# Kernel tuning notes

Hardware: AMD Instinct MI355X
Metric: run time of the kernel (lower is better)

Reference implementation:

```python
import jax, jax.numpy as jnp
import numpy as np

N_NODES = 40000
N_EDGES = 640000
D_IN = 512
D_OUT = 128


def setup_inputs() -> dict:
    key = jax.random.key(0)
    k_x, k_w, k_a, k_v, k_r, k_c = jax.random.split(key, 6)
    # Xavier-uniform bound for Linear(in=512, out=128)
    bound = float(np.sqrt(6.0 / (D_IN + D_OUT)))
    x = jax.random.normal(k_x, (N_NODES, D_IN), dtype=jnp.float32)
    weight = jax.random.uniform(k_w, (D_OUT, D_IN), dtype=jnp.float32,
                                minval=-bound, maxval=bound)
    bias = jnp.zeros((D_OUT,), dtype=jnp.float32)
    # PReLU default init is 0.25 (single shared slope)
    alpha = jnp.full((1,), 0.25, dtype=jnp.float32)
    edge_val = jax.random.uniform(k_v, (N_EDGES,), dtype=jnp.float32)
    edge_row = jax.random.randint(k_r, (N_EDGES,), 0, N_NODES, dtype=jnp.int32)
    edge_col = jax.random.randint(k_c, (N_EDGES,), 0, N_NODES, dtype=jnp.int32)
    return {"x": x, "weight": weight, "bias": bias, "alpha": alpha,
            "edge_val": edge_val, "edge_row": edge_row, "edge_col": edge_col}


def reference(x, weight, bias, alpha, edge_val, edge_row, edge_col):
    # seq = fc_1(input): [N, D_out]
    seq = jnp.einsum('ni,oi->no', x, weight)
    # torch.spmm(adj, seq) with adj in COO form:
    # out[r] = sum over edges (r, c, v) of v * seq[c]
    msgs = edge_val[:, None] * seq[edge_col]          # [E, D_out]
    agg = jax.ops.segment_sum(msgs, edge_row, num_segments=x.shape[0])
    agg = agg + bias
    # PReLU with a single shared slope alpha
    return jnp.where(agg > 0, agg, alpha[0] * agg)
```

## Files before the change

kernel.cpp:

```cpp
#include <hip/hip_runtime.h>
#include <hip/hip_bf16.h>

#define N_NODES 40000
#define N_EDGES 640000
#define D_IN 512
#define D_OUT 128
#define BM 128
#define BK 64
#define CAPC 32
#define OVF_MAX 4096
#define NB_GE 313
#define NB_SC 625
#define EPT 4

typedef __attribute__((ext_vector_type(4))) float f32x4;
typedef __attribute__((ext_vector_type(8))) short bf16x8;
typedef __attribute__((ext_vector_type(4))) unsigned short us4;

static __device__ __forceinline__ unsigned short f2bf(float f) {
    unsigned int u = __float_as_uint(f);
    unsigned int r = u + 0x7fffu + ((u >> 16) & 1u);
    return (unsigned short)(r >> 16);
}

__global__ __launch_bounds__(256) void prep_kernel(int4* __restrict__ zbase, int nz4)
{
    const int stride = 512 * 256;
    for (int i = blockIdx.x * 256 + threadIdx.x; i < nz4; i += stride)
        zbase[i] = make_int4(0, 0, 0, 0);
}

__global__ __launch_bounds__(256) void fused_kernel(
    const float* __restrict__ x, const float* __restrict__ w,
    unsigned short* __restrict__ seq,
    const int* __restrict__ erow, const int* __restrict__ ecol,
    const float* __restrict__ eval, int* __restrict__ cursor,
    unsigned int* __restrict__ bucket, int* __restrict__ ovf_cnt,
    int4* __restrict__ ovf)
{
    if (blockIdx.x >= NB_GE) {
        const int base = (blockIdx.x - NB_GE) * (256 * EPT) + threadIdx.x;
        int r[EPT], c[EPT];
        float v[EPT];
        #pragma unroll
        for (int j = 0; j < EPT; j++) {
            int e = base + j * 256;
            r[j] = erow[e]; c[j] = ecol[e]; v[j] = eval[e];
        }
        int slot[EPT];
        #pragma unroll
        for (int j = 0; j < EPT; j++) slot[j] = atomicAdd(&cursor[r[j]], 1);
        #pragma unroll
        for (int j = 0; j < EPT; j++) {
            if (slot[j] < CAPC) {
                bucket[(size_t)r[j] * CAPC + slot[j]] =
                    ((unsigned int)f2bf(v[j]) << 16) | (unsigned int)c[j];
            } else {
                int o = atomicAdd(ovf_cnt, 1);
                if (o < OVF_MAX)
                    ovf[o] = make_int4(r[j], c[j], __float_as_int(v[j]), 0);
            }
        }
        return;
    }

    __shared__ unsigned short As[BM * BK];
    __shared__ unsigned short Bs[D_OUT * BK];

    const int tid = threadIdx.x;
    const int lane = tid & 63;
    const int wv = tid >> 6;
    const int block_row = blockIdx.x * BM;
    const int srow = tid >> 3;
    const int scol = (tid & 7) * 8;

    f32x4 ra[4][2], rb[4][2];

    auto issue_loads = [&](int k0) {
        #pragma unroll
        for (int p = 0; p < 4; ++p) {
            int gr = block_row + srow + p * 32; if (gr >= N_NODES) gr = N_NODES - 1;
            const float* sa = x + (size_t)gr * D_IN + k0 + scol;
            ra[p][0] = *(const f32x4*)sa;
            ra[p][1] = *(const f32x4*)(sa + 4);
            const float* sb = w + (size_t)(srow + p * 32) * D_IN + k0 + scol;
            rb[p][0] = *(const f32x4*)sb;
            rb[p][1] = *(const f32x4*)(sb + 4);
        }
    };

    f32x4 acc[2][8];
    #pragma unroll
    for (int i = 0; i < 2; i++)
        #pragma unroll
        for (int j = 0; j < 8; j++)
            acc[i][j] = f32x4{0.f, 0.f, 0.f, 0.f};

    issue_loads(0);

    for (int kt = 0; kt < D_IN / BK; ++kt) {
        __syncthreads();
        #pragma unroll
        for (int p = 0; p < 4; ++p) {
            int r = srow + p * 32;
            us4 h0, h1, g0, g1;
            #pragma unroll
            for (int q = 0; q < 4; q++) {
                h0[q] = f2bf(ra[p][0][q]); h1[q] = f2bf(ra[p][1][q]);
                g0[q] = f2bf(rb[p][0][q]); g1[q] = f2bf(rb[p][1][q]);
            }
            int off = (r * (BK * 2) + scol * 2) ^ ((r & 7) << 4);
            *(us4*)((char*)As + off)     = h0;
            *(us4*)((char*)As + off + 8) = h1;
            *(us4*)((char*)Bs + off)     = g0;
            *(us4*)((char*)Bs + off + 8) = g1;
        }
        if (kt < D_IN / BK - 1) issue_loads((kt + 1) * BK);
        __syncthreads();

        #pragma unroll
        for (int ks = 0; ks < 2; ++ks) {
            const int kb = ks * 32 + (lane >> 4) * 8;
            bf16x8 a[2], b[8];
            #pragma unroll
            for (int m = 0; m < 2; m++) {
                int r = wv * 32 + m * 16 + (lane & 15);
                int off = (r * (BK * 2) + kb * 2) ^ ((r & 7) << 4);
                a[m] = *(const bf16x8*)((const char*)As + off);
            }
            #pragma unroll
            for (int n = 0; n < 8; n++) {
                int r = n * 16 + (lane & 15);
                int off = (r * (BK * 2) + kb * 2) ^ ((r & 7) << 4);
                b[n] = *(const bf16x8*)((const char*)Bs + off);
            }
            #pragma unroll
            for (int m = 0; m < 2; m++)
                #pragma unroll
                for (int n = 0; n < 8; n++)
                    acc[m][n] = __builtin_amdgcn_mfma_f32_16x16x32_bf16(a[m], b[n], acc[m][n], 0, 0, 0);
        }
    }

    #pragma unroll
    for (int m = 0; m < 2; m++) {
        #pragma unroll
        for (int r = 0; r < 4; r++) {
            int grow = block_row + wv * 32 + m * 16 + (lane >> 4) * 4 + r;
            if (grow < N_NODES) {
                #pragma unroll
                for (int n = 0; n < 8; n++) {
                    int col = n * 16 + (lane & 15);
                    seq[(size_t)grow * D_OUT + col] = f2bf(acc[m][n][r]);
                }
            }
        }
    }
}

__global__ __launch_bounds__(256) void agg_kernel(
    const unsigned short* __restrict__ seq, const int* __restrict__ cursor,
    const unsigned int* __restrict__ bucket, const int* __restrict__ ovf_cnt,
    const int4* __restrict__ ovf, const float* __restrict__ bias,
    const float* __restrict__ alpha, float* __restrict__ out)
{
    const int row = blockIdx.x * 4 + (threadIdx.x >> 6);
    const int lane = threadIdx.x & 63;

    int cnt = cursor[row];
    int mx = cnt < CAPC ? cnt : CAPC;
    const unsigned int* bk = bucket + (size_t)row * CAPC;

    float a0 = 0.f, a1 = 0.f;
    for (int s = 0; s < mx; s += 8) {
        #pragma unroll
        for (int j = 0; j < 8; j++) {
            unsigned int q = bk[s + j];
            float vv = __uint_as_float(q & 0xffff0000u);
            int col = q & 0xffff;
            unsigned int p = *(const unsigned int*)(seq + ((size_t)col << 7) + lane * 2);
            a0 += vv * __uint_as_float(p << 16);
            a1 += vv * __uint_as_float(p & 0xffff0000u);
        }
    }

    int on = *ovf_cnt;
    on = on < OVF_MAX ? on : OVF_MAX;
    for (int i = 0; i < on; ++i) {
        int4 t = ovf[i];
        if (t.x == row) {
            float vv = __int_as_float(t.z);
            unsigned int p = *(const unsigned int*)(seq + ((size_t)t.y << 7) + lane * 2);
            a0 += vv * __uint_as_float(p << 16);
            a1 += vv * __uint_as_float(p & 0xffff0000u);
        }
    }

    float al = alpha[0];
    float2 bi = *(const float2*)(bias + lane * 2);
    float r0 = a0 + bi.x;
    float r1 = a1 + bi.y;
    r0 = r0 > 0.f ? r0 : al * r0;
    r1 = r1 > 0.f ? r1 : al * r1;
    *(float2*)(out + (size_t)row * D_OUT + lane * 2) = make_float2(r0, r1);
}

extern "C" void kernel_launch(void* const* d_in, const int* in_sizes, int n_in,
                              void* d_out, int out_size, void* d_ws, size_t ws_size,
                              hipStream_t stream)
{
    (void)in_sizes; (void)n_in; (void)out_size; (void)ws_size;
    const float* x     = (const float*)d_in[0];
    const float* w     = (const float*)d_in[1];
    const float* bias  = (const float*)d_in[2];
    const float* alpha = (const float*)d_in[3];
    const float* eval  = (const float*)d_in[4];
    const int*   erow  = (const int*)d_in[5];
    const int*   ecol  = (const int*)d_in[6];
    float* out = (float*)d_out;

    char* ws = (char*)d_ws;
    unsigned short* seq  = (unsigned short*)ws;
    int*  cursor  = (int*)(ws + 10240000);
    int*  ovf_cnt = (int*)(ws + 10400000);
    int4* ovf     = (int4*)(ws + 10400016);
    unsigned int* bucket = (unsigned int*)(ws + 10465552);

    const int nz4 = 334097;
    prep_kernel<<<512, 256, 0, stream>>>((int4*)(ws + 10240000), nz4);
    fused_kernel<<<NB_GE + NB_SC, 256, 0, stream>>>(x, w, seq, erow, ecol, eval,
                                                    cursor, bucket, ovf_cnt, ovf);
    agg_kernel<<<N_NODES / 4, 256, 0, stream>>>(seq, cursor, bucket, ovf_cnt, ovf,
                                                bias, alpha, out);
}
```

Before: 189.2 us.

## Replace atomic COO bucketing with atomic-free hashed slots plus verify pass

Edge scatter now writes edge ids into a 64-slot per-row table indexed by the low bits of the edge id, with no atomics. A new verify kernel detects edges whose slot was overwritten by a collision and routes them to a small atomic secondary bucket or an overflow list. Aggregation walks the slot table via a ballot mask and gathers col/val through the edge ids. This trades the atomic cursor contention for an extra kernel launch, a zeroed table more than twice the size, and indirect ecol/eval loads in the aggregation loop.

```diff
diff --git a/kernel.cpp b/kernel.cpp
--- a/kernel.cpp
+++ b/kernel.cpp
@@ -7,11 +7,12 @@
 #define D_OUT 128
 #define BM 128
 #define BK 64
-#define CAPC 32
-#define OVF_MAX 4096
+#define CAP1 64
+#define CAP2 12
+#define OVF_MAX 8192
 #define NB_GE 313
-#define NB_SC 625
-#define EPT 4
+#define NB_HS 313
+#define NB_VF 625
 
 typedef __attribute__((ext_vector_type(4))) float f32x4;
 typedef __attribute__((ext_vector_type(8))) short bf16x8;
@@ -33,32 +34,16 @@
 __global__ __launch_bounds__(256) void fused_kernel(
     const float* __restrict__ x, const float* __restrict__ w,
     unsigned short* __restrict__ seq,
-    const int* __restrict__ erow, const int* __restrict__ ecol,
-    const float* __restrict__ eval, int* __restrict__ cursor,
-    unsigned int* __restrict__ bucket, int* __restrict__ ovf_cnt,
-    int4* __restrict__ ovf)
+    const int* __restrict__ erow, unsigned int* __restrict__ bucket1)
 {
     if (blockIdx.x >= NB_GE) {
-        const int base = (blockIdx.x - NB_GE) * (256 * EPT) + threadIdx.x;
-        int r[EPT], c[EPT];
-        float v[EPT];
-        #pragma unroll
-        for (int j = 0; j < EPT; j++) {
+        const int base = (blockIdx.x - NB_GE) * 2048 + threadIdx.x;
+        #pragma unroll
+        for (int j = 0; j < 8; j++) {
             int e = base + j * 256;
-            r[j] = erow[e]; c[j] = ecol[e]; v[j] = eval[e];
-        }
-        int slot[EPT];
-        #pragma unroll
-        for (int j = 0; j < EPT; j++) slot[j] = atomicAdd(&cursor[r[j]], 1);
-        #pragma unroll
-        for (int j = 0; j < EPT; j++) {
-            if (slot[j] < CAPC) {
-                bucket[(size_t)r[j] * CAPC + slot[j]] =
-                    ((unsigned int)f2bf(v[j]) << 16) | (unsigned int)c[j];
-            } else {
-                int o = atomicAdd(ovf_cnt, 1);
-                if (o < OVF_MAX)
-                    ovf[o] = make_int4(r[j], c[j], __float_as_int(v[j]), 0);
+            if (e < N_EDGES) {
+                int r = erow[e];
+                bucket1[(size_t)r * CAP1 + (e & 63)] = (unsigned int)(e + 1);
             }
         }
         return;
@@ -158,24 +143,90 @@
     }
 }
 
+__global__ __launch_bounds__(256) void verify_kernel(
+    const int* __restrict__ erow, const int* __restrict__ ecol,
+    const float* __restrict__ eval, const unsigned int* __restrict__ bucket1,
+    int* __restrict__ cursor2, unsigned int* __restrict__ bucket2,
+    int* __restrict__ ovf_cnt, int4* __restrict__ ovf)
+{
+    const int base = blockIdx.x * 1024 + threadIdx.x;
+    int r[4];
+    unsigned int id[4];
+    #pragma unroll
+    for (int j = 0; j < 4; j++) {
+        int e = base + j * 256;
+        r[j] = erow[e];
+        id[j] = bucket1[(size_t)r[j] * CAP1 + (e & 63)];
+    }
+    #pragma unroll
+    for (int j = 0; j < 4; j++) {
+        int e = base + j * 256;
+        if (id[j] != (unsigned int)(e + 1)) {
+            int c = ecol[e];
+            float v = eval[e];
+            int s2 = atomicAdd(&cursor2[r[j]], 1);
+            if (s2 < CAP2) {
+                bucket2[(size_t)r[j] * CAP2 + s2] =
+                    ((unsigned int)f2bf(v) << 16) | (unsigned int)c;
+            } else {
+                int o = atomicAdd(ovf_cnt, 1);
+                if (o < OVF_MAX) ovf[o] = make_int4(r[j], c, __float_as_int(v), 0);
+            }
+        }
+    }
+}
+
 __global__ __launch_bounds__(256) void agg_kernel(
-    const unsigned short* __restrict__ seq, const int* __restrict__ cursor,
-    const unsigned int* __restrict__ bucket, const int* __restrict__ ovf_cnt,
-    const int4* __restrict__ ovf, const float* __restrict__ bias,
-    const float* __restrict__ alpha, float* __restrict__ out)
+    const unsigned short* __restrict__ seq, const int* __restrict__ ecol,
+    const float* __restrict__ eval, const unsigned int* __restrict__ bucket1,
+    const int* __restrict__ cursor2, const unsigned int* __restrict__ bucket2,
+    const int* __restrict__ ovf_cnt, const int4* __restrict__ ovf,
+    const float* __restrict__ bias, const float* __restrict__ alpha,
+    float* __restrict__ out)
 {
     const int row = blockIdx.x * 4 + (threadIdx.x >> 6);
     const int lane = threadIdx.x & 63;
 
-    int cnt = cursor[row];
-    int mx = cnt < CAPC ? cnt : CAPC;
-    const unsigned int* bk = bucket + (size_t)row * CAPC;
+    unsigned int myid = bucket1[(size_t)row * CAP1 + lane];
+    unsigned long long mask = __ballot(myid != 0);
 
     float a0 = 0.f, a1 = 0.f;
-    for (int s = 0; s < mx; s += 8) {
-        #pragma unroll
-        for (int j = 0; j < 8; j++) {
-            unsigned int q = bk[s + j];
+    while (mask) {
+        int b0 = __builtin_ctzll(mask); mask &= mask - 1;
+        int b1 = -1, b2 = -1, b3 = -1;
+        if (mask) { b1 = __builtin_ctzll(mask); mask &= mask - 1; }
+        if (mask) { b2 = __builtin_ctzll(mask); mask &= mask - 1; }
+        if (mask) { b3 = __builtin_ctzll(mask); mask &= mask - 1; }
+        int i0 = (int)__shfl(myid, b0) - 1;
+        int i1 = (int)__shfl(myid, b1 < 0 ? b0 : b1) - 1;
+        int i2 = (int)__shfl(myid, b2 < 0 ? b0 : b2) - 1;
+        int i3 = (int)__shfl(myid, b3 < 0 ? b0 : b3) - 1;
+        int c0 = ecol[i0], c1 = ecol[i1], c2 = ecol[i2], c3 = ecol[i3];
+        float v0 = eval[i0];
+        float v1 = b1 >= 0 ? eval[i1] : 0.f;
+        float v2 = b2 >= 0 ? eval[i2] : 0.f;
+        float v3 = b3 >= 0 ? eval[i3] : 0.f;
+        unsigned int p0 = *(const unsigned int*)(seq + ((size_t)c0 << 7) + lane * 2);
+        unsigned int p1 = *(const unsigned int*)(seq + ((size_t)c1 << 7) + lane * 2);
+        unsigned int p2 = *(const unsigned int*)(seq + ((size_t)c2 << 7) + lane * 2);
+        unsigned int p3 = *(const unsigned int*)(seq + ((size_t)c3 << 7) + lane * 2);
+        a0 += v0 * __uint_as_float(p0 << 16);
+        a1 += v0 * __uint_as_float(p0 & 0xffff0000u);
+        a0 += v1 * __uint_as_float(p1 << 16);
+        a1 += v1 * __uint_as_float(p1 & 0xffff0000u);
+        a0 += v2 * __uint_as_float(p2 << 16);
+        a1 += v2 * __uint_as_float(p2 & 0xffff0000u);
+        a0 += v3 * __uint_as_float(p3 << 16);
+        a1 += v3 * __uint_as_float(p3 & 0xffff0000u);
+    }
+
+    int cnt2 = cursor2[row];
+    int mx2 = cnt2 < CAP2 ? cnt2 : CAP2;
+    const unsigned int* bk2 = bucket2 + (size_t)row * CAP2;
+    for (int s = 0; s < mx2; s += 4) {
+        #pragma unroll
+        for (int j = 0; j < 4; j++) {
+            unsigned int q = bk2[s + j];
             float vv = __uint_as_float(q & 0xffff0000u);
             int col = q & 0xffff;
             unsigned int p = *(const unsigned int*)(seq + ((size_t)col << 7) + lane * 2);
@@ -220,16 +271,18 @@
     float* out = (float*)d_out;
 
     char* ws = (char*)d_ws;
-    unsigned short* seq  = (unsigned short*)ws;
-    int*  cursor  = (int*)(ws + 10240000);
-    int*  ovf_cnt = (int*)(ws + 10400000);
-    int4* ovf     = (int4*)(ws + 10400016);
-    unsigned int* bucket = (unsigned int*)(ws + 10465552);
-
-    const int nz4 = 334097;
+    unsigned short* seq     = (unsigned short*)ws;
+    unsigned int*   bucket1 = (unsigned int*)(ws + 10240000);
+    unsigned int*   bucket2 = (unsigned int*)(ws + 20480000);
+    int*  cursor2 = (int*)(ws + 22400000);
+    int*  ovf_cnt = (int*)(ws + 22560000);
+    int4* ovf     = (int4*)(ws + 22560016);
+
+    const int nz4 = 778193;
     prep_kernel<<<512, 256, 0, stream>>>((int4*)(ws + 10240000), nz4);
-    fused_kernel<<<NB_GE + NB_SC, 256, 0, stream>>>(x, w, seq, erow, ecol, eval,
-                                                    cursor, bucket, ovf_cnt, ovf);
-    agg_kernel<<<N_NODES / 4, 256, 0, stream>>>(seq, cursor, bucket, ovf_cnt, ovf,
-                                                bias, alpha, out);
-}
+    fused_kernel<<<NB_GE + NB_HS, 256, 0, stream>>>(x, w, seq, erow, bucket1);
+    verify_kernel<<<NB_VF, 256, 0, stream>>>(erow, ecol, eval, bucket1,
+                                             cursor2, bucket2, ovf_cnt, ovf);
+    agg_kernel<<<N_NODES / 4, 256, 0, stream>>>(seq, ecol, eval, bucket1, cursor2,
+                                                bucket2, ovf_cnt, ovf, bias, alpha, out);
+}
```

Result: slower. 215.1 us (+13.7%).
